# Performance work log

Measured on AMD Instinct MI355X. Metric: run time of the kernel, lower is better.

The kernel has to match this reference:

```python
import jax, jax.numpy as jnp
import numpy as np

DIM = 512
HEADS = 8
HEAD_DIM = DIM // HEADS
SCALE = HEAD_DIM ** -0.5
LN_EPS = 1e-5


def _layernorm(t, g, b):
    mu = jnp.mean(t, axis=-1, keepdims=True)
    var = jnp.mean(jnp.square(t - mu), axis=-1, keepdims=True)
    return (t - mu) * jax.lax.rsqrt(var + LN_EPS) * g + b


def setup_inputs() -> dict:
    key = jax.random.key(0)
    ks = jax.random.split(key, 8)
    B, C, H, W = 2, DIM, 48, 48
    s = 1.0 / np.sqrt(DIM)
    return {
        "x": jax.random.normal(ks[0], (B, C, H, W), jnp.float32),
        "y": jax.random.normal(ks[1], (B, C, H, W), jnp.float32),
        # linear weights stored [in, out]
        "k_w": jax.random.uniform(ks[2], (DIM, DIM), jnp.float32, -s, s),
        "k_b": jax.random.uniform(ks[3], (DIM,), jnp.float32, -s, s),
        "qv_w": jax.random.uniform(ks[4], (DIM, 2 * DIM), jnp.float32, -s, s),
        "qv_b": jax.random.uniform(ks[5], (2 * DIM,), jnp.float32, -s, s),
        "lnx_g": jnp.ones((DIM,), jnp.float32),
        "lnx_b": jnp.zeros((DIM,), jnp.float32),
        "lny_g": jnp.ones((DIM,), jnp.float32),
        "lny_b": jnp.zeros((DIM,), jnp.float32),
    }


def _split_qv(t, qv_w, qv_b):
    B, N, C = t.shape
    qv = (t @ qv_w + qv_b).reshape(B, N, 2, HEADS, HEAD_DIM)
    qv = jnp.transpose(qv, (2, 0, 3, 1, 4))  # [2, B, h, N, d]
    return qv[0], qv[1]


def _heads(t):
    B, N, C = t.shape
    return jnp.transpose(t.reshape(B, N, HEADS, HEAD_DIM), (0, 2, 1, 3))  # [B,h,N,d]


def reference(x, y, k_w, k_b, qv_w, qv_b, lnx_g, lnx_b, lny_g, lny_b):
    B, C = x.shape[0], x.shape[1]
    xf = _layernorm(jnp.transpose(x.reshape(B, C, -1), (0, 2, 1)), lnx_g, lnx_b)  # [B,N,C]
    yf = _layernorm(jnp.transpose(y.reshape(B, C, -1), (0, 2, 1)), lny_g, lny_b)
    N = xf.shape[1]

    y_q, y_v = _split_qv(yf, qv_w, qv_b)
    x_q, x_v = _split_qv(xf, qv_w, qv_b)
    y_k = _heads(yf @ k_w + k_b)
    x_k = _heads(xf @ k_w + k_b)

    # branch 1: softmax(x_q y_k^T) x_v  -> standard [B,N,C]
    a1 = jax.nn.softmax(jnp.einsum('bhnd,bhmd->bhnm', x_q, y_k) * SCALE, axis=-1)
    xo = jnp.einsum('bhnm,bhmd->bhnd', a1, x_v)
    xo = jnp.transpose(xo, (0, 2, 1, 3)).reshape(B, N, C)

    # branch 2: faithful reproduction of torch quirk (x_k kept a leading 1-dim,
    # so the output [1,B,h,N,d].transpose(1,2).reshape(B,N,C) scrambles layout)
    a2 = jax.nn.softmax(jnp.einsum('bhnd,bhmd->bhnm', y_q, x_k) * SCALE, axis=-1)
    yo = jnp.einsum('bhnm,bhmd->bhnd', a2, y_v)  # [B,h,N,d]
    yo = jnp.transpose(yo[None], (0, 2, 1, 3, 4)).reshape(B, N, C)

    return jnp.concatenate([xo, yo], axis=0)  # [2B, N, C]
```

## Files before the change

kernel.cpp:

```cpp
#include <hip/hip_runtime.h>

#define DIM 512
#define NTOK 2304
#define HEADS 8
#define HD 64
#define LN_EPS 1e-5f
#define BNC 2359296
#define QSC 0.18033688011112042f

typedef __attribute__((ext_vector_type(8))) short short8;
typedef __attribute__((ext_vector_type(4))) short sh4;
typedef __attribute__((ext_vector_type(4))) float f32x4;

__device__ __forceinline__ short f2bf(float f) {
    union { float f; unsigned u; } x; x.f = f;
    unsigned r = (x.u + 0x7fffu + ((x.u >> 16) & 1u)) >> 16;
    return (short)(r & 0xffffu);
}
__device__ __forceinline__ unsigned fbits(float f) {
    union { float f; unsigned u; } x; x.f = f; return x.u;
}
__device__ __forceinline__ void gl2lds(const short* g, short* l) {
    __builtin_amdgcn_global_load_lds(
        (const __attribute__((address_space(1))) unsigned int*)g,
        (__attribute__((address_space(3))) unsigned int*)l, 16, 0, 0);
}

__global__ void k_pre(const float* __restrict__ x, const float* __restrict__ y,
                      const float* __restrict__ qv_w, const float* __restrict__ k_w,
                      const float* __restrict__ qv_b, const float* __restrict__ k_b,
                      const float* __restrict__ gx, const float* __restrict__ bx,
                      const float* __restrict__ gy, const float* __restrict__ by,
                      short* __restrict__ T, short* __restrict__ Wt,
                      float* __restrict__ bias) {
    __shared__ __align__(16) float tile[64][65];
    __shared__ float pS[4][64], pQ[4][64];
    __shared__ float muL[64], rsL[64];
    int bkid = blockIdx.x, tid = threadIdx.x;
    if (bkid < 1152) {
        int nt = bkid % 36, ct = (bkid / 36) % 8, sb = bkid / 288;
        int s = sb >> 1, b = sb & 1;
        int n0 = nt * 64, c0 = ct * 64;
        const float* src = (s ? y : x) + (size_t)b * DIM * NTOK;
        int nl = tid & 63, part = tid >> 6;
        {
            const float* p = src + n0 + nl;
            float sum = 0.f, sq = 0.f;
            for (int c = part * 128; c < part * 128 + 128; c++) {
                float v = p[(size_t)c * NTOK];
                sum += v; sq += v * v;
            }
            pS[part][nl] = sum; pQ[part][nl] = sq;
        }
        __syncthreads();
        if (tid < 64) {
            float ts = pS[0][tid] + pS[1][tid] + pS[2][tid] + pS[3][tid];
            float tq = pQ[0][tid] + pQ[1][tid] + pQ[2][tid] + pQ[3][tid];
            float m = ts * (1.0f / DIM);
            float var = tq * (1.0f / DIM) - m * m;
            muL[tid] = m;
            rsL[tid] = rsqrtf(var + LN_EPS);
        }
        for (int slot = tid; slot < 1024; slot += 256) {
            int r = slot >> 4, q = slot & 15;
            const float* p = src + (size_t)(c0 + r) * NTOK + n0 + q * 4;
            float4 v = *(const float4*)p;
            tile[r][q*4+0] = v.x; tile[r][q*4+1] = v.y;
            tile[r][q*4+2] = v.z; tile[r][q*4+3] = v.w;
        }
        __syncthreads();
        const float* g  = s ? gy : gx;
        const float* be = s ? by : bx;
        int nr = tid >> 2, cg = tid & 3;
        float m = muL[nr], r_ = rsL[nr];
        short8 o0, o1;
        for (int i = 0; i < 8; i++) {
            int c = c0 + cg * 16 + i;
            o0[i] = f2bf((tile[cg*16+i][nr] - m) * r_ * g[c] + be[c]);
        }
        for (int i = 0; i < 8; i++) {
            int c = c0 + cg * 16 + 8 + i;
            o1[i] = f2bf((tile[cg*16+8+i][nr] - m) * r_ * g[c] + be[c]);
        }
        short* dst = T + ((size_t)sb * NTOK + n0 + nr) * DIM + c0 + cg * 16;
        *(short8*)dst = o0;
        *(short8*)(dst + 8) = o1;
        return;
    }
    int idx = bkid - 1152;
    int jt = idx % 24, ct = idx / 24;
    int j0 = jt * 64, c0 = ct * 64;
    if (ct == 0 && tid < 64) {
        int j = j0 + tid;
        bias[j] = (j < 1024) ? qv_b[j] : k_b[j - 1024];
    }
    for (int slot = tid; slot < 1024; slot += 256) {
        int r = slot >> 4, q = slot & 15;
        int c = c0 + r;
        float4 v;
        if (j0 < 1024) v = *(const float4*)(qv_w + (size_t)c * 1024 + j0 + q * 4);
        else           v = *(const float4*)(k_w  + (size_t)c * 512  + (j0 - 1024) + q * 4);
        tile[r][q*4+0] = v.x; tile[r][q*4+1] = v.y;
        tile[r][q*4+2] = v.z; tile[r][q*4+3] = v.w;
    }
    __syncthreads();
    int jr = tid >> 2, cg = tid & 3;
    short8 o0, o1;
    for (int i = 0; i < 8; i++) o0[i] = f2bf(tile[cg*16+i][jr]);
    for (int i = 0; i < 8; i++) o1[i] = f2bf(tile[cg*16+8+i][jr]);
    short* dst = Wt + (size_t)(j0 + jr) * DIM + c0 + cg * 16;
    *(short8*)dst = o0;
    *(short8*)(dst + 8) = o1;
}

__global__ void __launch_bounds__(256)
k_gemm(const short* __restrict__ T, const short* __restrict__ Wt,
       const float* __restrict__ bias, short* __restrict__ QVK,
       short* __restrict__ VT) {
    __shared__ __align__(16) short smem[2 * 128 * 64];
    short* As = smem;
    short* Bs = smem + 128 * 64;
    int n0 = blockIdx.x * 128, j0 = blockIdx.y * 128, sb = blockIdx.z;
    int tid = threadIdx.x;
    int w = tid >> 6, l = tid & 63;
    int wr = w >> 1, wc = w & 1;
    int lrow = l & 15, quad = l >> 4;
    int r_in = (l >> 3) & 7, cc = l & 7;
    int ch = cc ^ r_in;
    int sw0 = (quad ^ (lrow & 7)) * 8;
    const short* Ab = T + (size_t)sb * NTOK * DIM;
    f32x4 acc[4][4] = {};
    for (int kk = 0; kk < 8; kk++) {
        if (kk) __syncthreads();
        for (int inst = 0; inst < 4; inst++) {
            int R = w * 32 + inst * 8 + r_in;
            gl2lds(Ab + (size_t)(n0 + R) * 512 + kk * 64 + ch * 8,
                   &As[(w * 32 + inst * 8) * 64]);
            gl2lds(Wt + (size_t)(j0 + R) * 512 + kk * 64 + ch * 8,
                   &Bs[(w * 32 + inst * 8) * 64]);
        }
        __syncthreads();
        for (int c2 = 0; c2 < 2; c2++) {
            int off = c2 ? (sw0 ^ 32) : sw0;
            short8 af[4], bf[4];
            for (int i = 0; i < 4; i++)
                af[i] = *(const short8*)&As[(wr*64 + i*16 + lrow) * 64 + off];
            for (int j = 0; j < 4; j++)
                bf[j] = *(const short8*)&Bs[(wc*64 + j*16 + lrow) * 64 + off];
            for (int i = 0; i < 4; i++)
                for (int j = 0; j < 4; j++)
                    acc[i][j] = __builtin_amdgcn_mfma_f32_16x16x32_bf16(af[i], bf[j], acc[i][j], 0, 0, 0);
        }
    }
    if (j0 >= 512 && j0 < 1024) {
        __syncthreads();
        for (int i = 0; i < 4; i++)
            for (int j = 0; j < 4; j++) {
                int jloc = wc * 64 + j * 16 + lrow;
                float bv = bias[j0 + jloc];
                int nloc = wr * 64 + i * 16 + quad * 4;
                int c8 = nloc >> 3, half = (nloc >> 2) & 1;
                sh4 pk;
                for (int reg = 0; reg < 4; reg++) pk[reg] = f2bf(acc[i][j][reg] + bv);
                *(sh4*)&smem[jloc * 128 + ((c8 ^ (jloc & 15)) * 8) + half * 4] = pk;
            }
        __syncthreads();
        for (int slot = tid; slot < 2048; slot += 256) {
            int row = slot >> 4, seg = slot & 15;
            short8 v = *(const short8*)&smem[row * 128 + ((seg ^ (row & 15)) * 8)];
            *(short8*)(VT + ((size_t)sb * 512 + (j0 - 512) + row) * NTOK + n0 + seg * 8) = v;
        }
    } else {
        for (int i = 0; i < 4; i++)
            for (int j = 0; j < 4; j++) {
                int jj = j0 + wc * 64 + j * 16 + lrow;
                float bv = bias[jj];
                float sc = (jj < 512) ? QSC : 1.0f;
                for (int reg = 0; reg < 4; reg++) {
                    int n = n0 + wr * 64 + i * 16 + quad * 4 + reg;
                    QVK[((size_t)sb * NTOK + n) * 1536 + jj] = f2bf((acc[i][j][reg] + bv) * sc);
                }
            }
    }
}

__global__ void __launch_bounds__(256)
k_attn(const short* __restrict__ QVK, const short* __restrict__ VT,
       float* __restrict__ out) {
    __shared__ __align__(16) short Ks[64 * 64];
    __shared__ __align__(16) short Vs[64 * 64];
    __shared__ __align__(16) short Qs[64 * 64];
    int id = blockIdx.x;
    int xcd = id & 7, rem = id >> 3;
    int qt = rem % 36, yhi = rem / 36;
    int yb = yhi * 8 + xcd;
    int br = yb >> 4;
    int b  = (yb >> 3) & 1;
    int h  = yb & 7;
    int tid = threadIdx.x;
    int w = tid >> 6, l = tid & 63;
    int lrow = l & 15, quad = l >> 4;
    int r_in = (l >> 3) & 7, cc = l & 7;
    int ch = cc ^ r_in;
    int sw0 = (quad ^ (lrow & 7)) * 8;
    int n0 = qt * 64;
    const short* Qg = QVK + ((size_t)(br * 2 + b) * NTOK) * 1536 + h * 64;
    const short* Kg = QVK + ((size_t)((1 - br) * 2 + b) * NTOK) * 1536 + 1024 + h * 64;
    const short* Vg = VT + ((size_t)(br * 2 + b) * 512 + h * 64) * NTOK;

    for (int inst = 0; inst < 2; inst++) {
        int R = w * 16 + inst * 8 + r_in;
        gl2lds(Qg + (size_t)(n0 + R) * 1536 + ch * 8, &Qs[(w * 16 + inst * 8) * 64]);
    }
    __syncthreads();
    short8 bq0 = *(const short8*)&Qs[(w * 16 + lrow) * 64 + sw0];
    short8 bq1 = *(const short8*)&Qs[(w * 16 + lrow) * 64 + (sw0 ^ 32)];
    short* Pw = &Qs[w * 16 * 64];

    short8 ones;
    for (int i = 0; i < 8; i++) ones[i] = (short)0x3F80;

    f32x4 Oacc[4] = {};
    f32x4 lacc = {};

    for (int mt = 0; mt < 36; mt++) {
        int m0 = mt * 64;
        __syncthreads();
        for (int inst = 0; inst < 2; inst++) {
            int R = w * 16 + inst * 8 + r_in;
            int Rb = (w * 16 + inst * 8) * 64;
            gl2lds(Kg + (size_t)(m0 + R) * 1536 + ch * 8, &Ks[Rb]);
            gl2lds(Vg + (size_t)R * NTOK + m0 + ch * 8, &Vs[Rb]);
        }
        __syncthreads();

        for (int sub = 0; sub < 4; sub++) {
            short8 ak0 = *(const short8*)&Ks[(sub * 16 + lrow) * 64 + sw0];
            short8 ak1 = *(const short8*)&Ks[(sub * 16 + lrow) * 64 + (sw0 ^ 32)];
            f32x4 a = {};
            a = __builtin_amdgcn_mfma_f32_16x16x32_bf16(ak0, bq0, a, 0, 0, 0);
            a = __builtin_amdgcn_mfma_f32_16x16x32_bf16(ak1, bq1, a, 0, 0, 0);
            float p0 = exp2f(a[0]), p1 = exp2f(a[1]);
            float p2 = exp2f(a[2]), p3 = exp2f(a[3]);
            uint2 pk;
            pk.x = __builtin_amdgcn_perm(fbits(p1), fbits(p0), 0x07060302u);
            pk.y = __builtin_amdgcn_perm(fbits(p3), fbits(p2), 0x07060302u);
            *(uint2*)&Pw[lrow * 64 + (((2 * sub + (quad >> 1)) ^ (lrow & 7)) * 8) + (quad & 1) * 4] = pk;
        }

        short8 ap0 = *(const short8*)&Pw[lrow * 64 + sw0];
        short8 ap1 = *(const short8*)&Pw[lrow * 64 + (sw0 ^ 32)];
        lacc = __builtin_amdgcn_mfma_f32_16x16x32_bf16(ones, ap0, lacc, 0, 0, 0);
        lacc = __builtin_amdgcn_mfma_f32_16x16x32_bf16(ones, ap1, lacc, 0, 0, 0);
        for (int ddt = 0; ddt < 4; ddt++) {
            short8 av0 = *(const short8*)&Vs[(ddt * 16 + lrow) * 64 + sw0];
            short8 av1 = *(const short8*)&Vs[(ddt * 16 + lrow) * 64 + (sw0 ^ 32)];
            Oacc[ddt] = __builtin_amdgcn_mfma_f32_16x16x32_bf16(av0, ap0, Oacc[ddt], 0, 0, 0);
            Oacc[ddt] = __builtin_amdgcn_mfma_f32_16x16x32_bf16(av1, ap1, Oacc[ddt], 0, 0, 0);
        }
    }

    float linv = 1.f / lacc[0];
    int n = n0 + w * 16 + lrow;
    for (int ddt = 0; ddt < 4; ddt++) {
        float4 o;
        o.x = Oacc[ddt][0] * linv;
        o.y = Oacc[ddt][1] * linv;
        o.z = Oacc[ddt][2] * linv;
        o.w = Oacc[ddt][3] * linv;
        if (br == 0)
            *(float4*)&out[((size_t)b * NTOK + n) * 512 + h * 64 + ddt * 16 + quad * 4] = o;
        else
            *(float4*)&out[(size_t)BNC + ((size_t)(h * 2 + b) * NTOK + n) * 64 + ddt * 16 + quad * 4] = o;
    }
}

extern "C" void kernel_launch(void* const* d_in, const int* in_sizes, int n_in,
                              void* d_out, int out_size, void* d_ws, size_t ws_size,
                              hipStream_t stream) {
    const float* x     = (const float*)d_in[0];
    const float* y     = (const float*)d_in[1];
    const float* k_w   = (const float*)d_in[2];
    const float* k_b   = (const float*)d_in[3];
    const float* qv_w  = (const float*)d_in[4];
    const float* qv_b  = (const float*)d_in[5];
    const float* lnx_g = (const float*)d_in[6];
    const float* lnx_b = (const float*)d_in[7];
    const float* lny_g = (const float*)d_in[8];
    const float* lny_b = (const float*)d_in[9];
    float* out = (float*)d_out;

    char* ws = (char*)d_ws;
    float* bias = (float*)ws;
    short* T    = (short*)(ws + 6144);
    short* Wt   = T + 4718592;
    short* QVK  = Wt + 786432;
    short* VT   = QVK + 14155776;

    k_pre  <<<1344, 256, 0, stream>>>(x, y, qv_w, k_w, qv_b, k_b,
                                      lnx_g, lnx_b, lny_g, lny_b, T, Wt, bias);
    k_gemm <<<dim3(18, 12, 4), 256, 0, stream>>>(T, Wt, bias, QVK, VT);
    k_attn <<<1152, 256, 0, stream>>>(QVK, VT, out);
}
```

Measured before the change: 204.4 us.

## Register-prefetch K/V tiles and give each attention wave two query blocks

The attention kernel now runs 128 threads (2 waves), each handling 32 query rows as two 16-row blocks, so every K/V fragment read from LDS feeds twice as many MFMAs. K/V tiles for the next step are loaded into registers while the current tile is being computed, then written to LDS at the top of the next iteration. This replaces the direct global-to-LDS loads that were bracketed by two barriers. The intent is to hide global latency and cut LDS traffic per FLOP, at the cost of more registers per thread and fewer waves per block.

```diff
diff --git a/kernel.cpp b/kernel.cpp
--- a/kernel.cpp
+++ b/kernel.cpp
@@ -184,7 +184,7 @@
     }
 }
 
-__global__ void __launch_bounds__(256)
+__global__ void __launch_bounds__(128)
 k_attn(const short* __restrict__ QVK, const short* __restrict__ VT,
        float* __restrict__ out) {
     __shared__ __align__(16) short Ks[64 * 64];
@@ -208,70 +208,115 @@
     const short* Kg = QVK + ((size_t)((1 - br) * 2 + b) * NTOK) * 1536 + 1024 + h * 64;
     const short* Vg = VT + ((size_t)(br * 2 + b) * 512 + h * 64) * NTOK;
 
-    for (int inst = 0; inst < 2; inst++) {
-        int R = w * 16 + inst * 8 + r_in;
-        gl2lds(Qg + (size_t)(n0 + R) * 1536 + ch * 8, &Qs[(w * 16 + inst * 8) * 64]);
-    }
+    #pragma unroll
+    for (int j = 0; j < 4; j++) {
+        int R = w * 32 + j * 8 + r_in;
+        gl2lds(Qg + (size_t)(n0 + R) * 1536 + ch * 8, &Qs[(w * 32 + j * 8) * 64]);
+    }
+
+    const short* Kp = Kg + (size_t)(w * 32 + r_in) * 1536 + ch * 8;
+    const short* Vp = Vg + (size_t)(w * 32 + r_in) * NTOK + ch * 8;
+    int lds_base = (w * 32) * 64 + l * 8;
+
+    short8 kr[4], vr[4];
+    #pragma unroll
+    for (int j = 0; j < 4; j++) {
+        kr[j] = *(const short8*)(Kp + (size_t)(j * 8) * 1536);
+        vr[j] = *(const short8*)(Vp + (size_t)(j * 8) * NTOK);
+    }
+    const short* Kc = Kp + (size_t)64 * 1536;
+    const short* Vc = Vp + 64;
+
     __syncthreads();
-    short8 bq0 = *(const short8*)&Qs[(w * 16 + lrow) * 64 + sw0];
-    short8 bq1 = *(const short8*)&Qs[(w * 16 + lrow) * 64 + (sw0 ^ 32)];
-    short* Pw = &Qs[w * 16 * 64];
+    short8 bq[2][2];
+    #pragma unroll
+    for (int qb = 0; qb < 2; qb++) {
+        bq[qb][0] = *(const short8*)&Qs[(w * 32 + qb * 16 + lrow) * 64 + sw0];
+        bq[qb][1] = *(const short8*)&Qs[(w * 32 + qb * 16 + lrow) * 64 + (sw0 ^ 32)];
+    }
+    short* Pw = &Qs[(w * 32) * 64];
 
     short8 ones;
+    #pragma unroll
     for (int i = 0; i < 8; i++) ones[i] = (short)0x3F80;
 
-    f32x4 Oacc[4] = {};
-    f32x4 lacc = {};
+    f32x4 Oacc[2][4] = {};
+    f32x4 lacc[2] = {};
 
     for (int mt = 0; mt < 36; mt++) {
-        int m0 = mt * 64;
-        __syncthreads();
-        for (int inst = 0; inst < 2; inst++) {
-            int R = w * 16 + inst * 8 + r_in;
-            int Rb = (w * 16 + inst * 8) * 64;
-            gl2lds(Kg + (size_t)(m0 + R) * 1536 + ch * 8, &Ks[Rb]);
-            gl2lds(Vg + (size_t)R * NTOK + m0 + ch * 8, &Vs[Rb]);
-        }
-        __syncthreads();
-
+        __syncthreads();
+        #pragma unroll
+        for (int j = 0; j < 4; j++) {
+            *(short8*)&Ks[lds_base + j * 8 * 64] = kr[j];
+            *(short8*)&Vs[lds_base + j * 8 * 64] = vr[j];
+        }
+        __syncthreads();
+        if (mt + 1 < 36) {
+            #pragma unroll
+            for (int j = 0; j < 4; j++) {
+                kr[j] = *(const short8*)(Kc + (size_t)(j * 8) * 1536);
+                vr[j] = *(const short8*)(Vc + (size_t)(j * 8) * NTOK);
+            }
+        }
+        Kc += (size_t)64 * 1536;
+        Vc += 64;
+        __builtin_amdgcn_sched_barrier(0);
+
+        #pragma unroll
         for (int sub = 0; sub < 4; sub++) {
             short8 ak0 = *(const short8*)&Ks[(sub * 16 + lrow) * 64 + sw0];
             short8 ak1 = *(const short8*)&Ks[(sub * 16 + lrow) * 64 + (sw0 ^ 32)];
-            f32x4 a = {};
-            a = __builtin_amdgcn_mfma_f32_16x16x32_bf16(ak0, bq0, a, 0, 0, 0);
-            a = __builtin_amdgcn_mfma_f32_16x16x32_bf16(ak1, bq1, a, 0, 0, 0);
-            float p0 = exp2f(a[0]), p1 = exp2f(a[1]);
-            float p2 = exp2f(a[2]), p3 = exp2f(a[3]);
-            uint2 pk;
-            pk.x = __builtin_amdgcn_perm(fbits(p1), fbits(p0), 0x07060302u);
-            pk.y = __builtin_amdgcn_perm(fbits(p3), fbits(p2), 0x07060302u);
-            *(uint2*)&Pw[lrow * 64 + (((2 * sub + (quad >> 1)) ^ (lrow & 7)) * 8) + (quad & 1) * 4] = pk;
-        }
-
-        short8 ap0 = *(const short8*)&Pw[lrow * 64 + sw0];
-        short8 ap1 = *(const short8*)&Pw[lrow * 64 + (sw0 ^ 32)];
-        lacc = __builtin_amdgcn_mfma_f32_16x16x32_bf16(ones, ap0, lacc, 0, 0, 0);
-        lacc = __builtin_amdgcn_mfma_f32_16x16x32_bf16(ones, ap1, lacc, 0, 0, 0);
+            #pragma unroll
+            for (int qb = 0; qb < 2; qb++) {
+                f32x4 a = {};
+                a = __builtin_amdgcn_mfma_f32_16x16x32_bf16(ak0, bq[qb][0], a, 0, 0, 0);
+                a = __builtin_amdgcn_mfma_f32_16x16x32_bf16(ak1, bq[qb][1], a, 0, 0, 0);
+                float p0 = exp2f(a[0]), p1 = exp2f(a[1]);
+                float p2 = exp2f(a[2]), p3 = exp2f(a[3]);
+                uint2 pk;
+                pk.x = __builtin_amdgcn_perm(fbits(p1), fbits(p0), 0x07060302u);
+                pk.y = __builtin_amdgcn_perm(fbits(p3), fbits(p2), 0x07060302u);
+                *(uint2*)&Pw[(qb * 16 + lrow) * 64 +
+                             (((2 * sub + (quad >> 1)) ^ (lrow & 7)) * 8) + (quad & 1) * 4] = pk;
+            }
+        }
+
+        short8 ap[2][2];
+        #pragma unroll
+        for (int qb = 0; qb < 2; qb++) {
+            ap[qb][0] = *(const short8*)&Pw[(qb * 16 + lrow) * 64 + sw0];
+            ap[qb][1] = *(const short8*)&Pw[(qb * 16 + lrow) * 64 + (sw0 ^ 32)];
+            lacc[qb] = __builtin_amdgcn_mfma_f32_16x16x32_bf16(ones, ap[qb][0], lacc[qb], 0, 0, 0);
+            lacc[qb] = __builtin_amdgcn_mfma_f32_16x16x32_bf16(ones, ap[qb][1], lacc[qb], 0, 0, 0);
+        }
+        #pragma unroll
         for (int ddt = 0; ddt < 4; ddt++) {
             short8 av0 = *(const short8*)&Vs[(ddt * 16 + lrow) * 64 + sw0];
             short8 av1 = *(const short8*)&Vs[(ddt * 16 + lrow) * 64 + (sw0 ^ 32)];
-            Oacc[ddt] = __builtin_amdgcn_mfma_f32_16x16x32_bf16(av0, ap0, Oacc[ddt], 0, 0, 0);
-            Oacc[ddt] = __builtin_amdgcn_mfma_f32_16x16x32_bf16(av1, ap1, Oacc[ddt], 0, 0, 0);
-        }
-    }
-
-    float linv = 1.f / lacc[0];
-    int n = n0 + w * 16 + lrow;
-    for (int ddt = 0; ddt < 4; ddt++) {
-        float4 o;
-        o.x = Oacc[ddt][0] * linv;
-        o.y = Oacc[ddt][1] * linv;
-        o.z = Oacc[ddt][2] * linv;
-        o.w = Oacc[ddt][3] * linv;
-        if (br == 0)
-            *(float4*)&out[((size_t)b * NTOK + n) * 512 + h * 64 + ddt * 16 + quad * 4] = o;
-        else
-            *(float4*)&out[(size_t)BNC + ((size_t)(h * 2 + b) * NTOK + n) * 64 + ddt * 16 + quad * 4] = o;
+            #pragma unroll
+            for (int qb = 0; qb < 2; qb++) {
+                Oacc[qb][ddt] = __builtin_amdgcn_mfma_f32_16x16x32_bf16(av0, ap[qb][0], Oacc[qb][ddt], 0, 0, 0);
+                Oacc[qb][ddt] = __builtin_amdgcn_mfma_f32_16x16x32_bf16(av1, ap[qb][1], Oacc[qb][ddt], 0, 0, 0);
+            }
+        }
+    }
+
+    #pragma unroll
+    for (int qb = 0; qb < 2; qb++) {
+        float linv = 1.f / lacc[qb][0];
+        int n = n0 + w * 32 + qb * 16 + lrow;
+        #pragma unroll
+        for (int ddt = 0; ddt < 4; ddt++) {
+            float4 o;
+            o.x = Oacc[qb][ddt][0] * linv;
+            o.y = Oacc[qb][ddt][1] * linv;
+            o.z = Oacc[qb][ddt][2] * linv;
+            o.w = Oacc[qb][ddt][3] * linv;
+            if (br == 0)
+                *(float4*)&out[((size_t)b * NTOK + n) * 512 + h * 64 + ddt * 16 + quad * 4] = o;
+            else
+                *(float4*)&out[(size_t)BNC + ((size_t)(h * 2 + b) * NTOK + n) * 64 + ddt * 16 + quad * 4] = o;
+        }
     }
 }
 
@@ -300,5 +345,5 @@
     k_pre  <<<1344, 256, 0, stream>>>(x, y, qv_w, k_w, qv_b, k_b,
                                       lnx_g, lnx_b, lny_g, lny_b, T, Wt, bias);
     k_gemm <<<dim3(18, 12, 4), 256, 0, stream>>>(T, Wt, bias, QVK, VT);
-    k_attn <<<1152, 256, 0, stream>>>(QVK, VT, out);
-}
+    k_attn <<<1152, 128, 0, stream>>>(QVK, VT, out);
+}
```

Result: slower. 225.6 us (+10.4%).

## Split attention over key halves and add register-prefetched K/V staging with combine kernel

Applied to the files above, without the earlier changes.

Splits the attention key dimension into two halves processed by separate blocks, doubling the grid so more waves run concurrently, and adds a k_norm kernel that sums the partial outputs and row sums and then normalises. It also replaces direct global-to-LDS loads with register prefetch of the next K/V tile, which overlaps global loads with MFMA work. The cost is extra partial-output traffic through workspace and one more kernel launch. Softmax still skips max subtraction, which is safe here because the partials are summed unnormalised.

```diff
diff --git a/kernel.cpp b/kernel.cpp
--- a/kernel.cpp
+++ b/kernel.cpp
@@ -186,12 +186,15 @@
 
 __global__ void __launch_bounds__(256)
 k_attn(const short* __restrict__ QVK, const short* __restrict__ VT,
-       float* __restrict__ out) {
+       float* __restrict__ out, float* __restrict__ O1,
+       float* __restrict__ l0, float* __restrict__ l1) {
     __shared__ __align__(16) short Ks[64 * 64];
     __shared__ __align__(16) short Vs[64 * 64];
     __shared__ __align__(16) short Qs[64 * 64];
     int id = blockIdx.x;
-    int xcd = id & 7, rem = id >> 3;
+    int half = id / 1152;
+    int rid = id % 1152;
+    int xcd = rid & 7, rem = rid >> 3;
     int qt = rem % 36, yhi = rem / 36;
     int yb = yhi * 8 + xcd;
     int br = yb >> 4;
@@ -204,6 +207,7 @@
     int ch = cc ^ r_in;
     int sw0 = (quad ^ (lrow & 7)) * 8;
     int n0 = qt * 64;
+    int m_base = half * 1152;
     const short* Qg = QVK + ((size_t)(br * 2 + b) * NTOK) * 1536 + h * 64;
     const short* Kg = QVK + ((size_t)((1 - br) * 2 + b) * NTOK) * 1536 + 1024 + h * 64;
     const short* Vg = VT + ((size_t)(br * 2 + b) * 512 + h * 64) * NTOK;
@@ -212,6 +216,22 @@
         int R = w * 16 + inst * 8 + r_in;
         gl2lds(Qg + (size_t)(n0 + R) * 1536 + ch * 8, &Qs[(w * 16 + inst * 8) * 64]);
     }
+
+    const short* KgA = Kg + (size_t)(m_base + w * 16 + r_in) * 1536 + ch * 8;
+    const short* KgB = Kg + (size_t)(m_base + w * 16 + 8 + r_in) * 1536 + ch * 8;
+    const short* VgA = Vg + (size_t)(w * 16 + r_in) * NTOK + m_base + ch * 8;
+    const short* VgB = Vg + (size_t)(w * 16 + 8 + r_in) * NTOK + m_base + ch * 8;
+    int lds_off = l * 8;
+
+    short8 ka = *(const short8*)(KgA);
+    short8 kb = *(const short8*)(KgB);
+    short8 va = *(const short8*)(VgA);
+    short8 vb = *(const short8*)(VgB);
+    const short* Kc = KgA + (size_t)64 * 1536;
+    const short* Kd = KgB + (size_t)64 * 1536;
+    const short* Vc = VgA + 64;
+    const short* Vd = VgB + 64;
+
     __syncthreads();
     short8 bq0 = *(const short8*)&Qs[(w * 16 + lrow) * 64 + sw0];
     short8 bq1 = *(const short8*)&Qs[(w * 16 + lrow) * 64 + (sw0 ^ 32)];
@@ -223,16 +243,24 @@
     f32x4 Oacc[4] = {};
     f32x4 lacc = {};
 
-    for (int mt = 0; mt < 36; mt++) {
-        int m0 = mt * 64;
-        __syncthreads();
-        for (int inst = 0; inst < 2; inst++) {
-            int R = w * 16 + inst * 8 + r_in;
-            int Rb = (w * 16 + inst * 8) * 64;
-            gl2lds(Kg + (size_t)(m0 + R) * 1536 + ch * 8, &Ks[Rb]);
-            gl2lds(Vg + (size_t)R * NTOK + m0 + ch * 8, &Vs[Rb]);
-        }
-        __syncthreads();
+    for (int mt = 0; mt < 18; mt++) {
+        __syncthreads();
+        *(short8*)&Ks[(w * 16)     * 64 + lds_off] = ka;
+        *(short8*)&Ks[(w * 16 + 8) * 64 + lds_off] = kb;
+        *(short8*)&Vs[(w * 16)     * 64 + lds_off] = va;
+        *(short8*)&Vs[(w * 16 + 8) * 64 + lds_off] = vb;
+        __syncthreads();
+        if (mt + 1 < 18) {
+            ka = *(const short8*)(Kc);
+            kb = *(const short8*)(Kd);
+            va = *(const short8*)(Vc);
+            vb = *(const short8*)(Vd);
+        }
+        Kc += (size_t)64 * 1536;
+        Kd += (size_t)64 * 1536;
+        Vc += 64;
+        Vd += 64;
+        __builtin_amdgcn_sched_barrier(0);
 
         for (int sub = 0; sub < 4; sub++) {
             short8 ak0 = *(const short8*)&Ks[(sub * 16 + lrow) * 64 + sw0];
@@ -260,19 +288,54 @@
         }
     }
 
-    float linv = 1.f / lacc[0];
     int n = n0 + w * 16 + lrow;
+    if (quad == 0) (half ? l1 : l0)[yb * NTOK + n] = lacc[0];
     for (int ddt = 0; ddt < 4; ddt++) {
         float4 o;
-        o.x = Oacc[ddt][0] * linv;
-        o.y = Oacc[ddt][1] * linv;
-        o.z = Oacc[ddt][2] * linv;
-        o.w = Oacc[ddt][3] * linv;
-        if (br == 0)
-            *(float4*)&out[((size_t)b * NTOK + n) * 512 + h * 64 + ddt * 16 + quad * 4] = o;
-        else
-            *(float4*)&out[(size_t)BNC + ((size_t)(h * 2 + b) * NTOK + n) * 64 + ddt * 16 + quad * 4] = o;
-    }
+        o.x = Oacc[ddt][0];
+        o.y = Oacc[ddt][1];
+        o.z = Oacc[ddt][2];
+        o.w = Oacc[ddt][3];
+        if (half == 0) {
+            if (br == 0)
+                *(float4*)&out[((size_t)b * NTOK + n) * 512 + h * 64 + ddt * 16 + quad * 4] = o;
+            else
+                *(float4*)&out[(size_t)BNC + ((size_t)(h * 2 + b) * NTOK + n) * 64 + ddt * 16 + quad * 4] = o;
+        } else {
+            *(float4*)&O1[((size_t)yb * NTOK + n) * 64 + ddt * 16 + quad * 4] = o;
+        }
+    }
+}
+
+__global__ void __launch_bounds__(256)
+k_norm(float* __restrict__ out, const float* __restrict__ O1,
+       const float* __restrict__ l0, const float* __restrict__ l1) {
+    int i = blockIdx.x * 256 + threadIdx.x;
+    int o = i * 4;
+    int yb, n, d;
+    if (o < BNC) {
+        int b = o / (NTOK * 512);
+        int r = o % (NTOK * 512);
+        n = r >> 9;
+        int c = r & 511;
+        d = c & 63;
+        yb = b * 8 + (c >> 6);
+    } else {
+        int o2 = o - BNC;
+        int hb = o2 / (NTOK * 64);
+        n = (o2 >> 6) % NTOK;
+        d = o2 & 63;
+        yb = 16 + (hb & 1) * 8 + (hb >> 1);
+    }
+    int li = yb * NTOK + n;
+    float linv = 1.f / (l0[li] + l1[li]);
+    float4 a = *(const float4*)&out[o];
+    float4 q = *(const float4*)&O1[(size_t)li * 64 + d];
+    a.x = (a.x + q.x) * linv;
+    a.y = (a.y + q.y) * linv;
+    a.z = (a.z + q.z) * linv;
+    a.w = (a.w + q.w) * linv;
+    *(float4*)&out[o] = a;
 }
 
 extern "C" void kernel_launch(void* const* d_in, const int* in_sizes, int n_in,
@@ -296,9 +359,13 @@
     short* Wt   = T + 4718592;
     short* QVK  = Wt + 786432;
     short* VT   = QVK + 14155776;
+    float* O1   = (float*)(ws + 48764928);
+    float* l0   = (float*)(ws + 67639296);
+    float* l1   = (float*)(ws + 67934208);
 
     k_pre  <<<1344, 256, 0, stream>>>(x, y, qv_w, k_w, qv_b, k_b,
                                       lnx_g, lnx_b, lny_g, lny_b, T, Wt, bias);
     k_gemm <<<dim3(18, 12, 4), 256, 0, stream>>>(T, Wt, bias, QVK, VT);
-    k_attn <<<1152, 256, 0, stream>>>(QVK, VT, out);
-}
+    k_attn <<<2304, 256, 0, stream>>>(QVK, VT, out, O1, l0, l1);
+    k_norm <<<4608, 256, 0, stream>>>(out, O1, l0, l1);
+}
```

New measurement: 202.3 us. About the same (-1.1%).
